# Kernel tuning notes

Hardware: AMD Instinct MI355X
Metric: run time of the kernel (lower is better)

The kernel has to match this reference:

```python
import jax, jax.numpy as jnp
import numpy as np

WS = 7          # window_size
HEADS = 6
HEAD_DIM = 32
DISP = WS // 2  # displacement = 3
NEG = -1e9      # stands in for -inf in shift masks (safe for grads/low precision)


def _rel_indices():
    # get_relative_distances(window_size) + window_size - 1
    pos = np.array([[i, j] for i in range(WS) for j in range(WS)])  # (49, 2)
    return pos[None, :, :] - pos[:, None, :] + WS - 1               # (49, 49, 2)


def _shift_mask(nw_h, nw_w):
    # per-window additive mask replicating upper_lower_mask / left_right_mask placement
    n = WS * WS
    ul = np.zeros((n, n), np.float32)
    ul[-DISP * WS:, :-DISP * WS] = NEG
    ul[:-DISP * WS, -DISP * WS:] = NEG
    m4 = np.zeros((WS, WS, WS, WS), np.float32)
    m4[:, -DISP:, :, :-DISP] = NEG
    m4[:, :-DISP, :, -DISP:] = NEG
    lr = m4.reshape(n, n)
    full = np.zeros((nw_h, nw_w, n, n), np.float32)
    full[-1, :] += ul              # dots[:, :, -nw_w:] += upper_lower_mask
    full[:, -1] += lr              # dots[:, :, nw_w-1::nw_w] += left_right_mask
    return full.reshape(nw_h * nw_w, n, n)


def setup_inputs() -> dict:
    key = jax.random.key(0)
    k1, k2, k3, k4 = jax.random.split(key, 4)
    dim, inner = 192, HEADS * HEAD_DIM
    return {
        "x": jax.random.normal(k1, (16, 56, 56, dim), jnp.float32),
        "w_qkv": jax.random.normal(k2, (dim, inner * 3), jnp.float32) * 0.02,
        "pos_embedding": jax.random.normal(k3, (2 * WS - 1, 2 * WS - 1), jnp.float32),
        "w_out": jax.random.normal(k4, (inner, dim), jnp.float32) * 0.02,
        "b_out": jnp.zeros((dim,), jnp.float32),
    }


def reference(x, w_qkv, pos_embedding, w_out, b_out):
    b, H, W, dim = x.shape
    nw_h, nw_w = H // WS, W // WS
    x = jnp.roll(x, (-DISP, -DISP), axis=(1, 2))          # shifted window
    qkv = x @ w_qkv                                       # [b,H,W,3*inner]
    q, k, v = jnp.split(qkv, 3, axis=-1)

    def to_windows(t):  # [b,H,W,inner] -> [b,h,nw,ws*ws,d]
        t = t.reshape(b, nw_h, WS, nw_w, WS, HEADS, HEAD_DIM)
        return t.transpose(0, 5, 1, 3, 2, 4, 6).reshape(b, HEADS, nw_h * nw_w, WS * WS, HEAD_DIM)

    q, k, v = to_windows(q), to_windows(k), to_windows(v)
    scale = HEAD_DIM ** -0.5
    dots = jnp.einsum('bhwid,bhwjd->bhwij', q, k) * scale  # [b,h,nw,49,49]

    rel = _rel_indices()
    bias = pos_embedding[rel[..., 0], rel[..., 1]]         # [49,49]
    dots = dots + bias
    dots = dots + jnp.asarray(_shift_mask(nw_h, nw_w))     # broadcast over b,h

    attn = jax.nn.softmax(dots, axis=-1)
    out = jnp.einsum('bhwij,bhwjd->bhwid', attn, v)        # [b,h,nw,49,d]
    out = out.reshape(b, HEADS, nw_h, nw_w, WS, WS, HEAD_DIM)
    out = out.transpose(0, 2, 4, 3, 5, 1, 6).reshape(b, H, W, HEADS * HEAD_DIM)
    out = out @ w_out + b_out
    return jnp.roll(out, (DISP, DISP), axis=(1, 2))
```

## Files before the change

### kernel.cpp

```cpp
#include <hip/hip_runtime.h>
#include <hip/hip_bf16.h>

typedef __bf16 bf16_t;
typedef __bf16 bf16x8 __attribute__((ext_vector_type(8)));
typedef float f32x4 __attribute__((ext_vector_type(4)));
typedef unsigned int u32;

#define NB 16
#define HW 56
#define DIM 192
#define N3 576
#define WS7 7
#define HEADS 6
#define HD 32
#define NTOK 49
#define MFMA(a, b, c) __builtin_amdgcn_mfma_f32_16x16x32_bf16(a, b, c, 0, 0, 0)

__device__ __forceinline__ void gld_lds16(const bf16_t* g, bf16_t* l) {
    __builtin_amdgcn_global_load_lds((const __attribute__((address_space(1))) u32*)g,
                                     (__attribute__((address_space(3))) u32*)l, 16, 0, 0);
}

__global__ __launch_bounds__(256) void prep_x_kernel(const float* __restrict__ x,
                                                     bf16_t* __restrict__ xb) {
    int idx = blockIdx.x * 256 + threadIdx.x;
    const int total = NB * HW * HW * (DIM / 8);
    if (idx >= total) return;
    int c8 = idx % (DIM / 8);
    int p  = idx / (DIM / 8);
    int xx = p % HW;
    int yy = (p / HW) % HW;
    int bb = p / (HW * HW);
    int ys = yy + 3; if (ys >= HW) ys -= HW;
    int xs = xx + 3; if (xs >= HW) xs -= HW;
    const float* src = x + ((size_t)(bb * HW + ys) * HW + xs) * DIM + c8 * 8;
    float4 a0 = *reinterpret_cast<const float4*>(src);
    float4 a1 = *reinterpret_cast<const float4*>(src + 4);
    bf16x8 o;
    o[0] = (bf16_t)a0.x; o[1] = (bf16_t)a0.y; o[2] = (bf16_t)a0.z; o[3] = (bf16_t)a0.w;
    o[4] = (bf16_t)a1.x; o[5] = (bf16_t)a1.y; o[6] = (bf16_t)a1.z; o[7] = (bf16_t)a1.w;
    *reinterpret_cast<bf16x8*>(xb + (size_t)idx * 8) = o;
}

__global__ __launch_bounds__(256) void prep_w_kernel(const float* __restrict__ wqkv,
                                                     const float* __restrict__ wout,
                                                     bf16_t* __restrict__ wqkvt,
                                                     bf16_t* __restrict__ woutt) {
    int idx = blockIdx.x * 256 + threadIdx.x;
    if (idx < N3 * DIM) {
        int k = idx % DIM, n = idx / DIM;
        wqkvt[idx] = (bf16_t)wqkv[(size_t)k * N3 + n];
    } else {
        int j = idx - N3 * DIM;
        if (j < DIM * DIM) {
            int k = j % DIM, n = j / DIM;
            woutt[j] = (bf16_t)wout[(size_t)k * DIM + n];
        }
    }
}

__global__ __launch_bounds__(256) void qkv_gemm2(const bf16_t* __restrict__ xb,
                                                 const bf16_t* __restrict__ wt,
                                                 bf16_t* __restrict__ qkv) {
    __shared__ alignas(16) bf16_t bsh[64 * DIM];
    const int mblk = blockIdx.x, nblk = blockIdx.y;
    const int wave = threadIdx.x >> 6, lane = threadIdx.x & 63;
    const int lo = lane & 15, hi = lane >> 4;

    const bf16_t* bt = wt + (size_t)nblk * 64 * DIM;
#pragma unroll
    for (int i = 0; i < 6; i++) {
        int s = wave * 384 + i * 64 + lane;
        int g = s ^ ((s / 24) & 7);
        gld_lds16(bt + g * 8, bsh + (wave * 384 + i * 64) * 8);
    }

    bf16x8 a[2][6];
    const bf16_t* ab = xb + ((size_t)mblk * 128 + wave * 32 + lo) * DIM + hi * 8;
#pragma unroll
    for (int mt = 0; mt < 2; mt++)
#pragma unroll
        for (int ks = 0; ks < 6; ks++)
            a[mt][ks] = *reinterpret_cast<const bf16x8*>(ab + mt * 16 * DIM + ks * 32);

    f32x4 acc[2][4];
#pragma unroll
    for (int mt = 0; mt < 2; mt++)
#pragma unroll
        for (int ct = 0; ct < 4; ct++) acc[mt][ct] = (f32x4){0.f, 0.f, 0.f, 0.f};

    __syncthreads();

#pragma unroll
    for (int ks = 0; ks < 6; ks++)
#pragma unroll
        for (int ct = 0; ct < 4; ct++) {
            int r = ct * 16 + lo;
            int off = (ks * 64 + hi * 16) ^ ((r & 7) << 4);
            bf16x8 b = *reinterpret_cast<const bf16x8*>((const char*)bsh + r * 384 + off);
            acc[0][ct] = MFMA(a[0][ks], b, acc[0][ct]);
            acc[1][ct] = MFMA(a[1][ks], b, acc[1][ct]);
        }

    const size_t rb = (size_t)mblk * 128 + wave * 32;
#pragma unroll
    for (int mt = 0; mt < 2; mt++)
#pragma unroll
        for (int ct = 0; ct < 4; ct++)
#pragma unroll
            for (int r = 0; r < 4; r++)
                qkv[(rb + mt * 16 + hi * 4 + r) * N3 + nblk * 64 + ct * 16 + lo] =
                    (bf16_t)acc[mt][ct][r];
}

__global__ __launch_bounds__(64) void attn_kernel2(const bf16_t* __restrict__ qkv,
                                                   const float* __restrict__ pe,
                                                   bf16_t* __restrict__ att) {
    const int win = blockIdx.x, h = blockIdx.y, bb = blockIdx.z;
    const int wh = win >> 3, ww = win & 7;
    const int lane = threadIdx.x;
    const int lo = lane & 15, hi = lane >> 4;

    __shared__ float pes[169];
    __shared__ bf16_t P[64][72];
    __shared__ alignas(16) bf16_t VT[32][72];

    for (int i = lane; i < 169; i += 64) pes[i] = pe[i];

    auto tokoff = [&](int t) -> size_t {
        int ti = t / 7, tj = t % 7;
        return ((size_t)(bb * HW + wh * WS7 + ti) * HW + ww * WS7 + tj) * N3 + h * HD;
    };

    {
        const int t = lane;
        bf16x8 v[4];
        if (t < NTOK) {
            const bf16_t* vp = qkv + tokoff(t) + 2 * DIM;
#pragma unroll
            for (int c = 0; c < 4; c++) v[c] = *reinterpret_cast<const bf16x8*>(vp + c * 8);
        } else {
#pragma unroll
            for (int c = 0; c < 4; c++)
#pragma unroll
                for (int j = 0; j < 8; j++) v[c][j] = (bf16_t)0.f;
        }
#pragma unroll
        for (int c = 0; c < 4; c++)
#pragma unroll
            for (int j = 0; j < 8; j++) VT[c * 8 + j][t] = v[c][j];
    }
    __syncthreads();

    bf16x8 qf[4], kf[4];
#pragma unroll
    for (int t4 = 0; t4 < 4; t4++) {
        int t = t4 * 16 + lo;
        if (t < NTOK) {
            size_t off = tokoff(t) + hi * 8;
            qf[t4] = *reinterpret_cast<const bf16x8*>(qkv + off);
            kf[t4] = *reinterpret_cast<const bf16x8*>(qkv + off + DIM);
        } else {
#pragma unroll
            for (int j = 0; j < 8; j++) { qf[t4][j] = (bf16_t)0.f; kf[t4][j] = (bf16_t)0.f; }
        }
    }

    const f32x4 zero4 = {0.f, 0.f, 0.f, 0.f};
    f32x4 s[4][4];
#pragma unroll
    for (int mt = 0; mt < 4; mt++)
#pragma unroll
        for (int ct = 0; ct < 4; ct++)
            s[mt][ct] = MFMA(qf[mt], kf[ct], zero4);

    const float scale = 0.17677669529663687f;
    const bool maskrow = (wh == 7), maskcol = (ww == 7);
    float rinv[4][4];
#pragma unroll
    for (int mt = 0; mt < 4; mt++) {
#pragma unroll
        for (int r = 0; r < 4; r++) {
            int ti = mt * 16 + hi * 4 + r;
            int yi = ti / 7, xi = ti % 7;
            float vals[4];
            float mx = -3e38f;
#pragma unroll
            for (int ct = 0; ct < 4; ct++) {
                int tj = ct * 16 + lo;
                float v = -1e30f;
                if (ti < NTOK && tj < NTOK) {
                    int yj = tj / 7, xj = tj % 7;
                    v = s[mt][ct][r] * scale + pes[(yj - yi + 6) * 13 + (xj - xi + 6)];
                    if (maskrow && ((yi >= 4) != (yj >= 4))) v = -1e30f;
                    if (maskcol && ((xi >= 4) != (xj >= 4))) v = -1e30f;
                }
                vals[ct] = v;
                mx = fmaxf(mx, v);
            }
#pragma unroll
            for (int off = 1; off < 16; off <<= 1) mx = fmaxf(mx, __shfl_xor(mx, off));
            float sum = 0.f;
#pragma unroll
            for (int ct = 0; ct < 4; ct++) {
                float p = __expf(vals[ct] - mx);
                sum += p;
                P[ti][ct * 16 + lo] = (bf16_t)p;
            }
#pragma unroll
            for (int off = 1; off < 16; off <<= 1) sum += __shfl_xor(sum, off);
            rinv[mt][r] = 1.f / sum;
        }
    }
    __syncthreads();

    f32x4 o[4][2];
#pragma unroll
    for (int mt = 0; mt < 4; mt++)
#pragma unroll
        for (int c2 = 0; c2 < 2; c2++) o[mt][c2] = zero4;

#pragma unroll
    for (int ks = 0; ks < 2; ks++) {
        bf16x8 vb[2];
#pragma unroll
        for (int c2 = 0; c2 < 2; c2++)
            vb[c2] = *reinterpret_cast<const bf16x8*>(&VT[c2 * 16 + lo][ks * 32 + hi * 8]);
#pragma unroll
        for (int mt = 0; mt < 4; mt++) {
            bf16x8 pa = *reinterpret_cast<const bf16x8*>(&P[mt * 16 + lo][ks * 32 + hi * 8]);
#pragma unroll
            for (int c2 = 0; c2 < 2; c2++)
                o[mt][c2] = MFMA(pa, vb[c2], o[mt][c2]);
        }
    }

#pragma unroll
    for (int mt = 0; mt < 4; mt++) {
#pragma unroll
        for (int r = 0; r < 4; r++) {
            int ti = mt * 16 + hi * 4 + r;
            if (ti < NTOK) {
                int y = wh * WS7 + ti / 7, x = ww * WS7 + ti % 7;
                size_t aoff = ((size_t)(bb * HW + y) * HW + x) * DIM + h * HD;
#pragma unroll
                for (int c2 = 0; c2 < 2; c2++)
                    att[aoff + c2 * 16 + lo] = (bf16_t)(o[mt][c2][r] * rinv[mt][r]);
            }
        }
    }
}

__global__ __launch_bounds__(256) void out_gemm2(const bf16_t* __restrict__ att,
                                                 const bf16_t* __restrict__ wt,
                                                 const float* __restrict__ bias,
                                                 float* __restrict__ out) {
    __shared__ alignas(16) bf16_t bsh[64 * DIM];
    const int mblk = blockIdx.x, nblk = blockIdx.y;
    const int wave = threadIdx.x >> 6, lane = threadIdx.x & 63;
    const int lo = lane & 15, hi = lane >> 4;

    const bf16_t* bt = wt + (size_t)nblk * 64 * DIM;
#pragma unroll
    for (int i = 0; i < 6; i++) {
        int s = wave * 384 + i * 64 + lane;
        int g = s ^ ((s / 24) & 7);
        gld_lds16(bt + g * 8, bsh + (wave * 384 + i * 64) * 8);
    }

    bf16x8 a[2][6];
    const bf16_t* ab = att + ((size_t)mblk * 128 + wave * 32 + lo) * DIM + hi * 8;
#pragma unroll
    for (int mt = 0; mt < 2; mt++)
#pragma unroll
        for (int ks = 0; ks < 6; ks++)
            a[mt][ks] = *reinterpret_cast<const bf16x8*>(ab + mt * 16 * DIM + ks * 32);

    f32x4 acc[2][4];
#pragma unroll
    for (int mt = 0; mt < 2; mt++)
#pragma unroll
        for (int ct = 0; ct < 4; ct++) acc[mt][ct] = (f32x4){0.f, 0.f, 0.f, 0.f};

    __syncthreads();

#pragma unroll
    for (int ks = 0; ks < 6; ks++)
#pragma unroll
        for (int ct = 0; ct < 4; ct++) {
            int r = ct * 16 + lo;
            int off = (ks * 64 + hi * 16) ^ ((r & 7) << 4);
            bf16x8 b = *reinterpret_cast<const bf16x8*>((const char*)bsh + r * 384 + off);
            acc[0][ct] = MFMA(a[0][ks], b, acc[0][ct]);
            acc[1][ct] = MFMA(a[1][ks], b, acc[1][ct]);
        }

    const int rb = mblk * 128 + wave * 32;
#pragma unroll
    for (int mt = 0; mt < 2; mt++)
#pragma unroll
        for (int r = 0; r < 4; r++) {
            int m = rb + mt * 16 + hi * 4 + r;
            int bb = m / (HW * HW);
            int rem = m - bb * HW * HW;
            int ya = rem / HW, xa = rem - ya * HW;
            int yo = ya + 3; if (yo >= HW) yo -= HW;
            int xo = xa + 3; if (xo >= HW) xo -= HW;
            size_t ob = ((size_t)(bb * HW + yo) * HW + xo) * DIM + nblk * 64;
#pragma unroll
            for (int ct = 0; ct < 4; ct++)
                out[ob + ct * 16 + lo] = acc[mt][ct][r] + bias[nblk * 64 + ct * 16 + lo];
        }
}

extern "C" void kernel_launch(void* const* d_in, const int* in_sizes, int n_in,
                              void* d_out, int out_size, void* d_ws, size_t ws_size,
                              hipStream_t stream) {
    const float* x    = (const float*)d_in[0];
    const float* wqkv = (const float*)d_in[1];
    const float* pe   = (const float*)d_in[2];
    const float* wout = (const float*)d_in[3];
    const float* bout = (const float*)d_in[4];
    float* out = (float*)d_out;

    char* ws = (char*)d_ws;
    const size_t XB_BYTES  = (size_t)NB * HW * HW * DIM * 2;
    const size_t QKV_BYTES = (size_t)NB * HW * HW * N3 * 2;
    const size_t ATT_BYTES = XB_BYTES;
    bf16_t* xb    = (bf16_t*)ws;
    bf16_t* qkv   = (bf16_t*)(ws + XB_BYTES);
    bf16_t* att   = (bf16_t*)(ws + XB_BYTES + QKV_BYTES);
    bf16_t* wqkvt = (bf16_t*)(ws + XB_BYTES + QKV_BYTES + ATT_BYTES);
    bf16_t* woutt = (bf16_t*)(ws + XB_BYTES + QKV_BYTES + ATT_BYTES + (size_t)N3 * DIM * 2);

    prep_x_kernel<<<(NB * HW * HW * (DIM / 8) + 255) / 256, 256, 0, stream>>>(x, xb);
    prep_w_kernel<<<(N3 * DIM + DIM * DIM + 255) / 256, 256, 0, stream>>>(wqkv, wout, wqkvt, woutt);
    qkv_gemm2<<<dim3(392, 9), 256, 0, stream>>>(xb, wqkvt, qkv);
    attn_kernel2<<<dim3(64, HEADS, NB), 64, 0, stream>>>(qkv, pe, att);
    out_gemm2<<<dim3(392, 3), 256, 0, stream>>>(att, woutt, bout, out);
}
```

Measured before the change: 175.8 us.

## Precompute bias/mask tables, fold scale into Q, enlarge QKV GEMM M-tile

Adds a small kernel that builds four 64x64 tables holding the positional bias plus shift mask, one per edge-window variant, so the attention softmax does a single table load per score instead of index arithmetic and mask checks. The softmax scale is folded into the Q columns when the QKV GEMM writes its output, removing a multiply in attention. The QKV GEMM now does 256 rows per block instead of 128, halving the grid and reusing each LDS B tile across more MFMAs, at the cost of more registers. The table reads come from global memory rather than LDS, and one leftover unused pointer expression remains.

```diff
diff --git a/kernel.cpp b/kernel.cpp
--- a/kernel.cpp
+++ b/kernel.cpp
@@ -59,7 +59,23 @@
     }
 }
 
-__global__ __launch_bounds__(256) void qkv_gemm2(const bf16_t* __restrict__ xb,
+__global__ __launch_bounds__(256) void prep_tbl_kernel(const float* __restrict__ pe,
+                                                       float* __restrict__ tbl) {
+    int idx = blockIdx.x * 256 + threadIdx.x;
+    if (idx >= 4 * 64 * 64) return;
+    int v = idx >> 12, rem = idx & 4095, ti = rem >> 6, tj = rem & 63;
+    float val = -1e9f;
+    if (ti < NTOK && tj < NTOK) {
+        int yi = ti / 7, xi = ti % 7, yj = tj / 7, xj = tj % 7;
+        val = pe[(yj - yi + 6) * 13 + (xj - xi + 6)];
+        bool mr = (v & 2) && ((yi >= 4) != (yj >= 4));
+        bool mc = (v & 1) && ((xi >= 4) != (xj >= 4));
+        if (mr || mc) val = -1e9f;
+    }
+    tbl[idx] = val;
+}
+
+__global__ __launch_bounds__(256) void qkv_gemm3(const bf16_t* __restrict__ xb,
                                                  const bf16_t* __restrict__ wt,
                                                  bf16_t* __restrict__ qkv) {
     __shared__ alignas(16) bf16_t bsh[64 * DIM];
@@ -75,17 +91,17 @@
         gld_lds16(bt + g * 8, bsh + (wave * 384 + i * 64) * 8);
     }
 
-    bf16x8 a[2][6];
-    const bf16_t* ab = xb + ((size_t)mblk * 128 + wave * 32 + lo) * DIM + hi * 8;
-#pragma unroll
-    for (int mt = 0; mt < 2; mt++)
+    bf16x8 a[4][6];
+    const bf16_t* ab = xb + ((size_t)mblk * 256 + wave * 64 + lo) * DIM + hi * 8;
+#pragma unroll
+    for (int mt = 0; mt < 4; mt++)
 #pragma unroll
         for (int ks = 0; ks < 6; ks++)
             a[mt][ks] = *reinterpret_cast<const bf16x8*>(ab + mt * 16 * DIM + ks * 32);
 
-    f32x4 acc[2][4];
-#pragma unroll
-    for (int mt = 0; mt < 2; mt++)
+    f32x4 acc[4][4];
+#pragma unroll
+    for (int mt = 0; mt < 4; mt++)
 #pragma unroll
         for (int ct = 0; ct < 4; ct++) acc[mt][ct] = (f32x4){0.f, 0.f, 0.f, 0.f};
 
@@ -98,34 +114,38 @@
             int r = ct * 16 + lo;
             int off = (ks * 64 + hi * 16) ^ ((r & 7) << 4);
             bf16x8 b = *reinterpret_cast<const bf16x8*>((const char*)bsh + r * 384 + off);
-            acc[0][ct] = MFMA(a[0][ks], b, acc[0][ct]);
-            acc[1][ct] = MFMA(a[1][ks], b, acc[1][ct]);
-        }
-
-    const size_t rb = (size_t)mblk * 128 + wave * 32;
-#pragma unroll
-    for (int mt = 0; mt < 2; mt++)
+#pragma unroll
+            for (int mt = 0; mt < 4; mt++)
+                acc[mt][ct] = MFMA(a[mt][ks], b, acc[mt][ct]);
+        }
+
+    const float qs = (nblk < 3) ? 0.17677669529663687f : 1.0f;
+    const size_t rb = (size_t)mblk * 256 + wave * 64;
+#pragma unroll
+    for (int mt = 0; mt < 4; mt++)
 #pragma unroll
         for (int ct = 0; ct < 4; ct++)
 #pragma unroll
             for (int r = 0; r < 4; r++)
                 qkv[(rb + mt * 16 + hi * 4 + r) * N3 + nblk * 64 + ct * 16 + lo] =
-                    (bf16_t)acc[mt][ct][r];
-}
-
-__global__ __launch_bounds__(64) void attn_kernel2(const bf16_t* __restrict__ qkv,
-                                                   const float* __restrict__ pe,
+                    (bf16_t)(acc[mt][ct][r] * qs);
+}
+
+__global__ __launch_bounds__(64) void attn_kernel3(const bf16_t* __restrict__ qkv,
+                                                   const float* __restrict__ tbl,
                                                    bf16_t* __restrict__ att) {
     const int win = blockIdx.x, h = blockIdx.y, bb = blockIdx.z;
     const int wh = win >> 3, ww = win & 7;
     const int lane = threadIdx.x;
     const int lo = lane & 15, hi = lane >> 4;
 
-    __shared__ float pes[169];
     __shared__ bf16_t P[64][72];
     __shared__ alignas(16) bf16_t VT[32][72];
 
-    for (int i = lane; i < 169; i += 64) pes[i] = pe[i];
+    const float* tv = tbl + (((wh == 7) ? 2 : 0 | 0) + ((wh == 7) ? 0 : 0), 0);
+    const int variant = ((wh == 7) ? 2 : 0) | ((ww == 7) ? 1 : 0);
+    const float* tbase = tbl + ((size_t)variant << 12);
+    (void)tv;
 
     auto tokoff = [&](int t) -> size_t {
         int ti = t / 7, tj = t % 7;
@@ -174,27 +194,18 @@
         for (int ct = 0; ct < 4; ct++)
             s[mt][ct] = MFMA(qf[mt], kf[ct], zero4);
 
-    const float scale = 0.17677669529663687f;
-    const bool maskrow = (wh == 7), maskcol = (ww == 7);
     float rinv[4][4];
 #pragma unroll
     for (int mt = 0; mt < 4; mt++) {
 #pragma unroll
         for (int r = 0; r < 4; r++) {
             int ti = mt * 16 + hi * 4 + r;
-            int yi = ti / 7, xi = ti % 7;
+            const float* trow = tbase + ti * 64 + lo;
             float vals[4];
             float mx = -3e38f;
 #pragma unroll
             for (int ct = 0; ct < 4; ct++) {
-                int tj = ct * 16 + lo;
-                float v = -1e30f;
-                if (ti < NTOK && tj < NTOK) {
-                    int yj = tj / 7, xj = tj % 7;
-                    v = s[mt][ct][r] * scale + pes[(yj - yi + 6) * 13 + (xj - xi + 6)];
-                    if (maskrow && ((yi >= 4) != (yj >= 4))) v = -1e30f;
-                    if (maskcol && ((xi >= 4) != (xj >= 4))) v = -1e30f;
-                }
+                float v = s[mt][ct][r] + trow[ct * 16];
                 vals[ct] = v;
                 mx = fmaxf(mx, v);
             }
@@ -327,15 +338,19 @@
     const size_t XB_BYTES  = (size_t)NB * HW * HW * DIM * 2;
     const size_t QKV_BYTES = (size_t)NB * HW * HW * N3 * 2;
     const size_t ATT_BYTES = XB_BYTES;
+    const size_t WQ_BYTES  = (size_t)N3 * DIM * 2;
+    const size_t WO_BYTES  = (size_t)DIM * DIM * 2;
     bf16_t* xb    = (bf16_t*)ws;
     bf16_t* qkv   = (bf16_t*)(ws + XB_BYTES);
     bf16_t* att   = (bf16_t*)(ws + XB_BYTES + QKV_BYTES);
     bf16_t* wqkvt = (bf16_t*)(ws + XB_BYTES + QKV_BYTES + ATT_BYTES);
-    bf16_t* woutt = (bf16_t*)(ws + XB_BYTES + QKV_BYTES + ATT_BYTES + (size_t)N3 * DIM * 2);
+    bf16_t* woutt = (bf16_t*)(ws + XB_BYTES + QKV_BYTES + ATT_BYTES + WQ_BYTES);
+    float*  tbl   = (float*)(ws + XB_BYTES + QKV_BYTES + ATT_BYTES + WQ_BYTES + WO_BYTES);
 
     prep_x_kernel<<<(NB * HW * HW * (DIM / 8) + 255) / 256, 256, 0, stream>>>(x, xb);
     prep_w_kernel<<<(N3 * DIM + DIM * DIM + 255) / 256, 256, 0, stream>>>(wqkv, wout, wqkvt, woutt);
-    qkv_gemm2<<<dim3(392, 9), 256, 0, stream>>>(xb, wqkvt, qkv);
-    attn_kernel2<<<dim3(64, HEADS, NB), 64, 0, stream>>>(qkv, pe, att);
+    prep_tbl_kernel<<<64, 256, 0, stream>>>(pe, tbl);
+    qkv_gemm3<<<dim3(196, 9), 256, 0, stream>>>(xb, wqkvt, qkv);
+    attn_kernel3<<<dim3(64, HEADS, NB), 64, 0, stream>>>(qkv, tbl, att);
     out_gemm2<<<dim3(392, 3), 256, 0, stream>>>(att, woutt, bout, out);
 }
```

New measurement: 180.3 us. 2.6% more time.
